# Kernel tuning notes

Measured on AMD Instinct MI355X. Metric: run time of the kernel, lower is better.

Reference implementation:

```python
import jax, jax.numpy as jnp
from jax import lax
import numpy as np

B, C, H, W, O, K = 2, 64, 256, 256, 64, 3
STRIDE, DIL = 1, 1


def setup_inputs() -> dict:
    key = jax.random.key(0)
    ks = jax.random.split(key, 6)
    x = jax.random.normal(ks[0], (B, C, H, W), jnp.float32)
    # offset-predicting conv: 2*k^2 output channels (y,x per kernel tap)
    offset_w = jax.random.normal(ks[1], (2 * K * K, C, K, K), jnp.float32) * 0.01
    offset_b = jax.random.normal(ks[2], (2 * K * K,), jnp.float32) * 0.01
    # modulation conv: k^2 output channels
    amp_w = jax.random.normal(ks[3], (K * K, C, K, K), jnp.float32) * 0.01
    amp_b = jax.random.normal(ks[4], (K * K,), jnp.float32) * 0.01
    # conv3d weight [O, C, 1, 1, k^2] flattened to [O, C, k^2]
    w3d = jax.random.normal(ks[5], (O, C, K * K), jnp.float32) * (1.0 / np.sqrt(C * K * K))
    return {"x": x, "offset_w": offset_w, "offset_b": offset_b,
            "amp_w": amp_w, "amp_b": amp_b, "w3d": w3d}


def _conv2d(inp, w, b):
    out = lax.conv_general_dilated(inp, w, (STRIDE, STRIDE), 'VALID')
    return out + b[None, :, None, None]


def reference(x, offset_w, offset_b, amp_w, amp_b, w3d):
    k2 = K * K
    # 'same' padding as _pad_intput (k=3, s=1, d=1 -> pad 1 each side)
    pfs = K + (K - 1) * (DIL - 1)
    p = pfs - 1
    p0 = p // 2
    pad = jnp.pad(x, ((0, 0), (0, 0), (p0, p - p0), (p0, p - p0)))
    Bb, Cc, in_h, in_w = pad.shape

    off = _conv2d(pad, offset_w, offset_b)          # [B, 2k2, oh, ow]
    oh, ow = off.shape[2], off.shape[3]
    off = off.reshape(Bb, k2, 2, oh, ow).transpose(0, 3, 4, 1, 2)  # [B,oh,ow,k2,2]
    y_off, x_off = off[..., 0], off[..., 1]

    amp = jax.nn.sigmoid(_conv2d(pad, amp_w, amp_b))  # [B, k2, oh, ow]

    # base sampling grid (row-major over (ky,kx), as in nn.Unfold)
    ky, kx = jnp.meshgrid(jnp.arange(K), jnp.arange(K), indexing='ij')
    yb = (jnp.arange(oh) * STRIDE)[:, None] + (ky.reshape(-1) * DIL)[None, :]  # [oh,k2]
    xb = (jnp.arange(ow) * STRIDE)[:, None] + (kx.reshape(-1) * DIL)[None, :]  # [ow,k2]

    y = jnp.clip(yb[None, :, None, :].astype(jnp.float32) + y_off, 0, in_h - 1)
    xx = jnp.clip(xb[None, None, :, :].astype(jnp.float32) + x_off, 0, in_w - 1)
    y0 = jnp.floor(y)
    x0 = jnp.floor(xx)
    y1 = jnp.clip(y0 + 1, 0, in_h - 1)
    x1 = jnp.clip(x0 + 1, 0, in_w - 1)
    y0 = jnp.clip(y0, 0, in_h - 1)
    x0 = jnp.clip(x0, 0, in_w - 1)

    flat = pad.transpose(0, 2, 3, 1).reshape(Bb, in_h * in_w, Cc)

    def gather(yi, xi):
        idx = (yi.astype(jnp.int32) * in_w + xi.astype(jnp.int32)).reshape(Bb, -1)
        return jnp.take_along_axis(flat, idx[:, :, None], axis=1).reshape(Bb, oh, ow, k2, Cc)

    p0g = gather(y0, x0)
    p1g = gather(y0, x1)
    p2g = gather(y1, x0)
    p3g = gather(y1, x1)

    w0 = (y1 - y) * (x1 - xx)
    w1 = (y1 - y) * (xx - x0)
    w2 = (y - y0) * (x1 - xx)
    w3 = (y - y0) * (xx - x0)
    pixels = (w0[..., None] * p0g + w1[..., None] * p1g +
              w2[..., None] * p2g + w3[..., None] * p3g)   # [B,oh,ow,k2,C]

    # sigmoid modulation
    pixels = pixels * amp.transpose(0, 2, 3, 1)[..., None]

    # conv3d (1,1,k^2), no bias: contract over C and k^2
    out = jnp.einsum('bhwkc,ock->bohw', pixels, w3d)
    return jax.nn.relu(out)
```

## Files before the change

### kernel.cpp

```cpp
#include <hip/hip_runtime.h>
#include <hip/hip_bf16.h>
#include <math.h>

#define BB 2
#define CC 64
#define HH 256
#define WW 256
#define OO 64
#define K2 9
#define HW 65536
#define CHW (CC*HW)

typedef _Float16 h8 __attribute__((ext_vector_type(8)));
typedef __fp16 fp16x2 __attribute__((ext_vector_type(2)));
typedef __attribute__((ext_vector_type(4))) unsigned int ux4;
typedef __attribute__((ext_vector_type(4))) float f32x4;

__device__ __forceinline__ int xcd_swz(int bid, int nwg) {
    const int per = nwg >> 3;
    return (bid & 7) * per + (bid >> 3);
}
__device__ __forceinline__ unsigned short f2h(float f) {
    _Float16 h = (_Float16)f;
    return __builtin_bit_cast(unsigned short, h);
}
__device__ __forceinline__ unsigned int pkrtz(float lo, float hi) {
    fp16x2 p = __builtin_amdgcn_cvt_pkrtz(lo, hi);
    return __builtin_bit_cast(unsigned int, p);
}
__device__ __forceinline__ h8 splat8(float f) {
    _Float16 h = (_Float16)f;
    h8 r = {h, h, h, h, h, h, h, h};
    return r;
}

__global__ __launch_bounds__(256) void k_prep(
    const float* __restrict__ offw, const float* __restrict__ ampw,
    const float* __restrict__ w3d,
    unsigned short* __restrict__ wA, unsigned short* __restrict__ wk)
{
    int i = blockIdx.x * 256 + threadIdx.x;
    if (i < 18432) {
        int ch = i / 576, sp = i % 576;
        int tap = sp >> 6, c = sp & 63;
        float v = 0.f;
        if (ch < 18)      v = offw[ch*576 + c*9 + tap];
        else if (ch < 27) v = ampw[(ch-18)*576 + c*9 + tap];
        wA[i] = f2h(v);
    } else if (i < 55296) {
        int j = i - 18432;
        int k = j >> 12, rem = j & 4095;
        int o = rem >> 6, c = rem & 63;
        wk[j] = f2h(w3d[o*576 + c*9 + k]);
    }
}

__global__ __launch_bounds__(256, 3) void k_fused(
    const float* __restrict__ x, const unsigned short* __restrict__ wA,
    const unsigned short* __restrict__ wk,
    const float* __restrict__ offb, const float* __restrict__ ampb,
    float* __restrict__ out)
{
    __shared__ __attribute__((aligned(16))) unsigned char lds[47200];
    unsigned char* tb = lds;
    _Float16* ot16 = (_Float16*)(lds + 43520);

    const int tid = threadIdx.x;
    const int idx = xcd_swz(blockIdx.x, BB*HH*4);
    const int wq = idx & 3, h = (idx >> 2) & 255, b = idx >> 10;
    const int w0 = wq << 6;
    const int lane = tid & 63, wv = tid >> 6;
    const int lrow = lane & 15, lg = lane >> 4;

    const float* xb = x + (size_t)b * CHW;
    const int r0a = h - 2, c0a = w0 - 2;

    {
        auto stage_plane = [&](int pp) {
            const int rr = pp / 68;
            const int cc = pp - rr*68;
            const int ra = r0a + rr, ca = c0a + cc;
            const bool inb = ((unsigned)ra < 256u) && ((unsigned)ca < 256u);
            const float* ps = xb + ra*256 + ca;
            const int swz = (pp & 7) << 4;
            float v[64];
#pragma unroll
            for (int j = 0; j < 64; ++j)
                v[j] = inb ? ps[(size_t)j * HW] : 0.f;
#pragma unroll
            for (int s = 0; s < 8; ++s) {
                ux4 w;
#pragma unroll
                for (int t = 0; t < 4; ++t)
                    w[t] = pkrtz(v[s*8 + 2*t], v[s*8 + 2*t + 1]);
                *(ux4*)(tb + pp*128 + ((s*16) ^ swz)) = w;
            }
        };
        stage_plane(tid);
        if (tid < 340 - 256) stage_plane(tid + 256);
    }
    __syncthreads();

    {
        f32x4 oacc0 = {0.f,0.f,0.f,0.f}, oacc1 = {0.f,0.f,0.f,0.f};
        const int pxl = wv*16 + lrow;
#pragma unroll
        for (int ks = 0; ks < 18; ++ks) {
            const int sbase = ks*32 + lg*8;
            const int tap = sbase >> 6;
            const int cb  = sbase & 63;
            const int ky = tap / 3, kx = tap - ky*3;
            const int pp = (ky + 1)*68 + pxl + kx + 1;
            const h8 bf = *(const h8*)(tb + pp*128 + ((2*cb) ^ ((pp & 7) << 4)));
            const h8 a0 = *(const h8*)(wA + (      lrow)*576 + sbase);
            const h8 a1 = *(const h8*)(wA + (16 + lrow)*576 + sbase);
            oacc0 = __builtin_amdgcn_mfma_f32_16x16x32_f16(a0, bf, oacc0, 0, 0, 0);
            oacc1 = __builtin_amdgcn_mfma_f32_16x16x32_f16(a1, bf, oacc1, 0, 0, 0);
        }
#pragma unroll
        for (int r = 0; r < 4; ++r) {
            int ch0 = lg*4 + r;
            ot16[ch0*68 + pxl] = (_Float16)(oacc0[r] + offb[ch0]);
            int ch1 = 16 + lg*4 + r;
            if (ch1 < 27) {
                float bias = (ch1 < 18) ? offb[ch1] : ampb[ch1 - 18];
                ot16[ch1*68 + pxl] = (_Float16)(oacc1[r] + bias);
            }
        }
    }
    __syncthreads();

    f32x4 acc[4];
#pragma unroll
    for (int n = 0; n < 4; ++n) acc[n] = (f32x4){0.f, 0.f, 0.f, 0.f};

    const int px = wv*16 + lrow;
    const int cA0 = lg*8;
    const int cA1 = 32 + lg*8;
    const int cb0 = lg*16;
    const int cb1 = 64 + lg*16;

#pragma unroll 3
    for (int k = 0; k < K2; ++k) {
        h8 bf0[4], bf1[4];
        {
            const unsigned short* wb = wk + (size_t)k*4096 + lg*8;
#pragma unroll
            for (int n = 0; n < 4; ++n) {
                bf0[n] = *(const h8*)(wb + (n*16 + lrow)*64);
                bf1[n] = *(const h8*)(wb + (n*16 + lrow)*64 + 32);
            }
        }

        const int ky = k / 3, kx = k - ky*3;
        const float oy = (float)ot16[(2*k  )*68 + px];
        const float ox = (float)ot16[(2*k+1)*68 + px];
        const float az = (float)ot16[(18+k )*68 + px];
        float yy = (float)(h + ky) + oy;
        float xx = (float)(w0 + px + kx) + ox;
        yy = fminf(fmaxf(yy, 0.f), 257.f);
        xx = fminf(fmaxf(xx, 0.f), 257.f);
        const float aa = 1.f / (1.f + __expf(-az));

        const float y0f = floorf(yy), x0f = floorf(xx);
        const float y1f = fminf(y0f + 1.f, 257.f);
        const float x1f = fminf(x0f + 1.f, 257.f);
        const float ay = yy - y0f, by = y1f - yy;
        const float ax = xx - x0f, bx = x1f - xx;
        const int r0 = (int)y0f - 1, r1 = (int)y1f - 1;
        const int c0 = (int)x0f - 1, c1 = (int)x1f - 1;
        const int rr0 = r0 - (h - 2), rr1 = r1 - (h - 2);
        const int cc0 = c0 - (w0 - 2), cc1 = c1 - (w0 - 2);
        const float w00 = by*bx*aa, w01 = by*ax*aa, w10 = ay*bx*aa, w11 = ay*ax*aa;

        h8 A0, A1;
        const bool ok = ((unsigned)rr0 <= 4u) && ((unsigned)rr1 <= 4u) &&
                        ((unsigned)cc0 <= 67u) && ((unsigned)cc1 <= 67u);
        if (ok) {
            const int pp00 = rr0*68 + cc0, pp01 = rr0*68 + cc1;
            const int pp10 = rr1*68 + cc0, pp11 = rr1*68 + cc1;
            const int s00 = (pp00 & 7) << 4, s01 = (pp01 & 7) << 4;
            const int s10 = (pp10 & 7) << 4, s11 = (pp11 & 7) << 4;
            const h8 Wb00 = splat8(w00), Wb01 = splat8(w01);
            const h8 Wb10 = splat8(w10), Wb11 = splat8(w11);

            auto bilerp8 = [&](int off) -> h8 {
                const h8 d00 = *(const h8*)(tb + pp00*128 + (off ^ s00));
                const h8 d01 = *(const h8*)(tb + pp01*128 + (off ^ s01));
                const h8 d10 = *(const h8*)(tb + pp10*128 + (off ^ s10));
                const h8 d11 = *(const h8*)(tb + pp11*128 + (off ^ s11));
                h8 t = d00 * Wb00;
                t = __builtin_elementwise_fma(d01, Wb01, t);
                t = __builtin_elementwise_fma(d10, Wb10, t);
                t = __builtin_elementwise_fma(d11, Wb11, t);
                return t;
            };
            A0 = bilerp8(cb0);
            A1 = bilerp8(cb1);
        } else {
            const bool vy0 = (unsigned)r0 < 256u, vy1 = (unsigned)r1 < 256u;
            const bool vx0 = (unsigned)c0 < 256u, vx1 = (unsigned)c1 < 256u;
            float W00 = w00, W01 = w01, W10 = w10, W11 = w11;
            int o00, o01, o10, o11;
            if (vy0 && vx0) o00 = r0*WW + c0; else { o00 = 0; W00 = 0.f; }
            if (vy0 && vx1) o01 = r0*WW + c1; else { o01 = 0; W01 = 0.f; }
            if (vy1 && vx0) o10 = r1*WW + c0; else { o10 = 0; W10 = 0.f; }
            if (vy1 && vx1) o11 = r1*WW + c1; else { o11 = 0; W11 = 0.f; }
            const float* pc0 = xb + (size_t)cA0 * HW;
            const float* pc1 = xb + (size_t)cA1 * HW;
#pragma unroll
            for (int jj = 0; jj < 8; ++jj) {
                float va = W00*pc0[o00] + W01*pc0[o01] + W10*pc0[o10] + W11*pc0[o11];
                pc0 += HW;
                A0[jj] = (_Float16)va;
                float vb = W00*pc1[o00] + W01*pc1[o01] + W10*pc1[o10] + W11*pc1[o11];
                pc1 += HW;
                A1[jj] = (_Float16)vb;
            }
        }

#pragma unroll
        for (int n = 0; n < 4; ++n)
            acc[n] = __builtin_amdgcn_mfma_f32_16x16x32_f16(A0, bf0[n], acc[n], 0, 0, 0);
#pragma unroll
        for (int n = 0; n < 4; ++n)
            acc[n] = __builtin_amdgcn_mfma_f32_16x16x32_f16(A1, bf1[n], acc[n], 0, 0, 0);
    }

    __syncthreads();
    float* ct = (float*)lds;
#pragma unroll
    for (int n = 0; n < 4; ++n)
#pragma unroll
        for (int r = 0; r < 4; ++r)
            ct[(n*16 + lrow)*66 + wv*16 + lg*4 + r] = acc[n][r];
    __syncthreads();

    const size_t ob = (size_t)b*OO*HW + (size_t)h*WW + w0;
#pragma unroll
    for (int it = 0; it < 16; ++it) {
        int o = it*4 + wv;
        out[ob + (size_t)o*HW + lane] = fmaxf(ct[o*66 + lane], 0.f);
    }
}

extern "C" void kernel_launch(void* const* d_in, const int* in_sizes, int n_in,
                              void* d_out, int out_size, void* d_ws, size_t ws_size,
                              hipStream_t stream) {
    const float* x    = (const float*)d_in[0];
    const float* offw = (const float*)d_in[1];
    const float* offb = (const float*)d_in[2];
    const float* ampw = (const float*)d_in[3];
    const float* ampb = (const float*)d_in[4];
    const float* w3d  = (const float*)d_in[5];
    float* out = (float*)d_out;

    unsigned short* wA = (unsigned short*)d_ws;
    unsigned short* wk = wA + 18432;

    k_prep<<<216, 256, 0, stream>>>(offw, ampw, w3d, wA, wk);
    k_fused<<<BB*HH*4, 256, 0, stream>>>(x, wA, wk, offb, ampb, out);
}
```

Baseline: 132.0 us.

## Process two output rows per block and software-pipeline weight fragment loads

Each block now covers a 2x64 output tile with 512 threads instead of 1x64 with 256. The staged halo grows from 5 to 6 rows, so the per-pixel halo traffic from global memory drops, and the bilinear in-tile check is widened to match. The tap loop is restructured to double-buffer the global weight fragments, issuing the next tap's loads before the current tap's compute to hide latency. LDS use and block size both grow, and the launch bound of 512 threads with 4 waves per EU may cap registers and limit occupancy.

```diff
diff --git a/kernel.cpp b/kernel.cpp
--- a/kernel.cpp
+++ b/kernel.cpp
@@ -55,62 +55,59 @@
     }
 }
 
-__global__ __launch_bounds__(256, 3) void k_fused(
+__global__ __launch_bounds__(512, 4) void k_fused(
     const float* __restrict__ x, const unsigned short* __restrict__ wA,
     const unsigned short* __restrict__ wk,
     const float* __restrict__ offb, const float* __restrict__ ampb,
     float* __restrict__ out)
 {
-    __shared__ __attribute__((aligned(16))) unsigned char lds[47200];
+    __shared__ __attribute__((aligned(16))) unsigned char lds[59360];
     unsigned char* tb = lds;
-    _Float16* ot16 = (_Float16*)(lds + 43520);
+    _Float16* ot16 = (_Float16*)(lds + 52224);
 
     const int tid = threadIdx.x;
-    const int idx = xcd_swz(blockIdx.x, BB*HH*4);
-    const int wq = idx & 3, h = (idx >> 2) & 255, b = idx >> 10;
-    const int w0 = wq << 6;
+    const int idx = xcd_swz(blockIdx.x, BB*(HH/2)*4);
+    const int wq = idx & 3, hp = (idx >> 2) & 127, b = idx >> 9;
+    const int h0 = hp << 1, w0 = wq << 6;
     const int lane = tid & 63, wv = tid >> 6;
     const int lrow = lane & 15, lg = lane >> 4;
 
     const float* xb = x + (size_t)b * CHW;
-    const int r0a = h - 2, c0a = w0 - 2;
-
-    {
-        auto stage_plane = [&](int pp) {
-            const int rr = pp / 68;
-            const int cc = pp - rr*68;
-            const int ra = r0a + rr, ca = c0a + cc;
-            const bool inb = ((unsigned)ra < 256u) && ((unsigned)ca < 256u);
-            const float* ps = xb + ra*256 + ca;
-            const int swz = (pp & 7) << 4;
-            float v[64];
-#pragma unroll
-            for (int j = 0; j < 64; ++j)
-                v[j] = inb ? ps[(size_t)j * HW] : 0.f;
-#pragma unroll
-            for (int s = 0; s < 8; ++s) {
-                ux4 w;
-#pragma unroll
-                for (int t = 0; t < 4; ++t)
-                    w[t] = pkrtz(v[s*8 + 2*t], v[s*8 + 2*t + 1]);
-                *(ux4*)(tb + pp*128 + ((s*16) ^ swz)) = w;
-            }
-        };
-        stage_plane(tid);
-        if (tid < 340 - 256) stage_plane(tid + 256);
+    const int r0a = h0 - 2, c0a = w0 - 2;
+
+    if (tid < 408) {
+        const int rr = tid / 68;
+        const int cc = tid - rr*68;
+        const int ra = r0a + rr, ca = c0a + cc;
+        const bool inb = ((unsigned)ra < 256u) && ((unsigned)ca < 256u);
+        const float* ps = xb + ra*256 + ca;
+        const int swz = (tid & 7) << 4;
+        float v[64];
+#pragma unroll
+        for (int j = 0; j < 64; ++j)
+            v[j] = inb ? ps[(size_t)j * HW] : 0.f;
+#pragma unroll
+        for (int s = 0; s < 8; ++s) {
+            ux4 w;
+#pragma unroll
+            for (int t = 0; t < 4; ++t)
+                w[t] = pkrtz(v[s*8 + 2*t], v[s*8 + 2*t + 1]);
+            *(ux4*)(tb + tid*128 + ((s*16) ^ swz)) = w;
+        }
     }
     __syncthreads();
 
     {
         f32x4 oacc0 = {0.f,0.f,0.f,0.f}, oacc1 = {0.f,0.f,0.f,0.f};
         const int pxl = wv*16 + lrow;
+        const int prow = pxl >> 6, pcol = pxl & 63;
 #pragma unroll
         for (int ks = 0; ks < 18; ++ks) {
             const int sbase = ks*32 + lg*8;
             const int tap = sbase >> 6;
             const int cb  = sbase & 63;
             const int ky = tap / 3, kx = tap - ky*3;
-            const int pp = (ky + 1)*68 + pxl + kx + 1;
+            const int pp = (prow + ky + 1)*68 + pcol + kx + 1;
             const h8 bf = *(const h8*)(tb + pp*128 + ((2*cb) ^ ((pp & 7) << 4)));
             const h8 a0 = *(const h8*)(wA + (      lrow)*576 + sbase);
             const h8 a1 = *(const h8*)(wA + (16 + lrow)*576 + sbase);
@@ -120,11 +117,11 @@
 #pragma unroll
         for (int r = 0; r < 4; ++r) {
             int ch0 = lg*4 + r;
-            ot16[ch0*68 + pxl] = (_Float16)(oacc0[r] + offb[ch0]);
+            ot16[ch0*132 + pxl] = (_Float16)(oacc0[r] + offb[ch0]);
             int ch1 = 16 + lg*4 + r;
             if (ch1 < 27) {
                 float bias = (ch1 < 18) ? offb[ch1] : ampb[ch1 - 18];
-                ot16[ch1*68 + pxl] = (_Float16)(oacc1[r] + bias);
+                ot16[ch1*132 + pxl] = (_Float16)(oacc1[r] + bias);
             }
         }
     }
@@ -135,29 +132,28 @@
     for (int n = 0; n < 4; ++n) acc[n] = (f32x4){0.f, 0.f, 0.f, 0.f};
 
     const int px = wv*16 + lrow;
+    const int prow = px >> 6, pcol = px & 63;
     const int cA0 = lg*8;
     const int cA1 = 32 + lg*8;
     const int cb0 = lg*16;
     const int cb1 = 64 + lg*16;
 
-#pragma unroll 3
-    for (int k = 0; k < K2; ++k) {
-        h8 bf0[4], bf1[4];
-        {
-            const unsigned short* wb = wk + (size_t)k*4096 + lg*8;
-#pragma unroll
-            for (int n = 0; n < 4; ++n) {
-                bf0[n] = *(const h8*)(wb + (n*16 + lrow)*64);
-                bf1[n] = *(const h8*)(wb + (n*16 + lrow)*64 + 32);
-            }
-        }
-
+    auto loadB = [&](int k, h8 f0[4], h8 f1[4]) {
+        const unsigned short* wb = wk + (size_t)k*4096 + lg*8;
+#pragma unroll
+        for (int n = 0; n < 4; ++n) {
+            f0[n] = *(const h8*)(wb + (n*16 + lrow)*64);
+            f1[n] = *(const h8*)(wb + (n*16 + lrow)*64 + 32);
+        }
+    };
+
+    auto tap_body = [&](int k, const h8 bf0[4], const h8 bf1[4]) {
         const int ky = k / 3, kx = k - ky*3;
-        const float oy = (float)ot16[(2*k  )*68 + px];
-        const float ox = (float)ot16[(2*k+1)*68 + px];
-        const float az = (float)ot16[(18+k )*68 + px];
-        float yy = (float)(h + ky) + oy;
-        float xx = (float)(w0 + px + kx) + ox;
+        const float oy = (float)ot16[(2*k  )*132 + px];
+        const float ox = (float)ot16[(2*k+1)*132 + px];
+        const float az = (float)ot16[(18+k )*132 + px];
+        float yy = (float)(h0 + prow + ky) + oy;
+        float xx = (float)(w0 + pcol + kx) + ox;
         yy = fminf(fmaxf(yy, 0.f), 257.f);
         xx = fminf(fmaxf(xx, 0.f), 257.f);
         const float aa = 1.f / (1.f + __expf(-az));
@@ -169,12 +165,12 @@
         const float ax = xx - x0f, bx = x1f - xx;
         const int r0 = (int)y0f - 1, r1 = (int)y1f - 1;
         const int c0 = (int)x0f - 1, c1 = (int)x1f - 1;
-        const int rr0 = r0 - (h - 2), rr1 = r1 - (h - 2);
-        const int cc0 = c0 - (w0 - 2), cc1 = c1 - (w0 - 2);
+        const int rr0 = r0 - r0a, rr1 = r1 - r0a;
+        const int cc0 = c0 - c0a, cc1 = c1 - c0a;
         const float w00 = by*bx*aa, w01 = by*ax*aa, w10 = ay*bx*aa, w11 = ay*ax*aa;
 
         h8 A0, A1;
-        const bool ok = ((unsigned)rr0 <= 4u) && ((unsigned)rr1 <= 4u) &&
+        const bool ok = ((unsigned)rr0 <= 5u) && ((unsigned)rr1 <= 5u) &&
                         ((unsigned)cc0 <= 67u) && ((unsigned)cc1 <= 67u);
         if (ok) {
             const int pp00 = rr0*68 + cc0, pp01 = rr0*68 + cc1;
@@ -225,7 +221,18 @@
 #pragma unroll
         for (int n = 0; n < 4; ++n)
             acc[n] = __builtin_amdgcn_mfma_f32_16x16x32_f16(A1, bf1[n], acc[n], 0, 0, 0);
-    }
+    };
+
+    h8 e0[4], e1[4], o0[4], o1[4];
+    loadB(0, e0, e1);
+#pragma unroll 1
+    for (int k = 0; k < 8; k += 2) {
+        loadB(k + 1, o0, o1);
+        tap_body(k, e0, e1);
+        loadB(k + 2, e0, e1);
+        tap_body(k + 1, o0, o1);
+    }
+    tap_body(8, e0, e1);
 
     __syncthreads();
     float* ct = (float*)lds;
@@ -233,14 +240,16 @@
     for (int n = 0; n < 4; ++n)
 #pragma unroll
         for (int r = 0; r < 4; ++r)
-            ct[(n*16 + lrow)*66 + wv*16 + lg*4 + r] = acc[n][r];
-    __syncthreads();
-
-    const size_t ob = (size_t)b*OO*HW + (size_t)h*WW + w0;
+            ct[(n*16 + lrow)*130 + wv*16 + lg*4 + r] = acc[n][r];
+    __syncthreads();
+
+    const size_t ob = (size_t)b*OO*HW + (size_t)h0*WW + w0;
 #pragma unroll
     for (int it = 0; it < 16; ++it) {
-        int o = it*4 + wv;
-        out[ob + (size_t)o*HW + lane] = fmaxf(ct[o*66 + lane], 0.f);
+        const int o = it*4 + (wv & 3);
+        const int row = wv >> 2;
+        out[ob + (size_t)o*HW + row*WW + lane] =
+            fmaxf(ct[o*130 + row*64 + lane], 0.f);
     }
 }
 
@@ -259,5 +268,5 @@
     unsigned short* wk = wA + 18432;
 
     k_prep<<<216, 256, 0, stream>>>(offw, ampw, w3d, wA, wk);
-    k_fused<<<BB*HH*4, 256, 0, stream>>>(x, wA, wk, offb, ampb, out);
-}
+    k_fused<<<BB*(HH/2)*4, 512, 0, stream>>>(x, wA, wk, offb, ampb, out);
+}
```

Result: slower. 171.2 us (+29.7%).

## Split fused kernel into transpose, offset-conv, and gather stages using padded NHWC fp16 copy

Applied to the files above, without the earlier changes.

Adds a pre-pass that transposes x into a zero-padded channels-last fp16 buffer in workspace. The offset/modulation conv becomes its own kernel writing fp16 offsets and sigmoid amplitudes to global memory. The main kernel then gathers bilinear samples straight from the global NHWC buffer with no LDS staging and no out-of-tile fallback path. This removes the per-block strided NCHW loads and the slow fallback path, at the cost of a memset, two extra launches and extra global round trips for the offsets.

```diff
diff --git a/kernel.cpp b/kernel.cpp
--- a/kernel.cpp
+++ b/kernel.cpp
@@ -11,6 +11,18 @@
 #define HW 65536
 #define CHW (CC*HW)
 
+#define XTW 258
+#define XT_ROW (XTW*64)
+#define XT_BATCH (XTW*XTW*64)
+
+#define WA_B   0u
+#define WK_B   36864u
+#define XT_B   110592u
+#define OU_B   17151076u
+#undef OU_B
+#define OU_B   17150976u
+#define AMP_B  21869568u
+
 typedef _Float16 h8 __attribute__((ext_vector_type(8)));
 typedef __fp16 fp16x2 __attribute__((ext_vector_type(2)));
 typedef __attribute__((ext_vector_type(4))) unsigned int ux4;
@@ -24,6 +36,9 @@
     _Float16 h = (_Float16)f;
     return __builtin_bit_cast(unsigned short, h);
 }
+__device__ __forceinline__ float h2f(unsigned short u) {
+    return (float)__builtin_bit_cast(_Float16, u);
+}
 __device__ __forceinline__ unsigned int pkrtz(float lo, float hi) {
     fp16x2 p = __builtin_amdgcn_cvt_pkrtz(lo, hi);
     return __builtin_bit_cast(unsigned int, p);
@@ -34,113 +49,146 @@
     return r;
 }
 
-__global__ __launch_bounds__(256) void k_prep(
-    const float* __restrict__ offw, const float* __restrict__ ampw,
-    const float* __restrict__ w3d,
-    unsigned short* __restrict__ wA, unsigned short* __restrict__ wk)
+__global__ __launch_bounds__(256) void k_pre(
+    const float* __restrict__ x, const float* __restrict__ offw,
+    const float* __restrict__ ampw, const float* __restrict__ w3d,
+    unsigned short* __restrict__ wA, unsigned short* __restrict__ wk,
+    unsigned short* __restrict__ xt)
 {
-    int i = blockIdx.x * 256 + threadIdx.x;
-    if (i < 18432) {
-        int ch = i / 576, sp = i % 576;
-        int tap = sp >> 6, c = sp & 63;
-        float v = 0.f;
-        if (ch < 18)      v = offw[ch*576 + c*9 + tap];
-        else if (ch < 27) v = ampw[(ch-18)*576 + c*9 + tap];
-        wA[i] = f2h(v);
-    } else if (i < 55296) {
-        int j = i - 18432;
-        int k = j >> 12, rem = j & 4095;
-        int o = rem >> 6, c = rem & 63;
-        wk[j] = f2h(w3d[o*576 + c*9 + k]);
-    }
-}
-
-__global__ __launch_bounds__(256, 3) void k_fused(
-    const float* __restrict__ x, const unsigned short* __restrict__ wA,
-    const unsigned short* __restrict__ wk,
+    const int tid = threadIdx.x;
+    const int id = blockIdx.x;
+    if (id < 512) {
+        __shared__ __attribute__((aligned(16))) unsigned char tl[32768];
+        const int b = id >> 8, h = id & 255;
+        const float* xb = x + (size_t)b*CHW + h*256;
+        const int wv = tid >> 6, lane = tid & 63;
+        for (int ip = 0; ip < 8; ++ip) {
+            const int c0 = wv*16 + ip*2;
+            const float* p0 = xb + (size_t)c0*HW;
+#pragma unroll
+            for (int j = 0; j < 4; ++j) {
+                const int px = j*64 + lane;
+                const float v0 = p0[px];
+                const float v1 = p0[HW + px];
+                *(unsigned int*)(tl + px*128 + ((2*c0) ^ ((px & 7) << 4))) =
+                    pkrtz(v0, v1);
+            }
+        }
+        __syncthreads();
+        const int lrow = lane & 15, lg = lane >> 4;
+        unsigned char* rowp = (unsigned char*)(xt + (size_t)b*XT_BATCH +
+                                               (size_t)(h+1)*XT_ROW + 64);
+#pragma unroll
+        for (int g = 0; g < 4; ++g) {
+            const int px = wv*64 + g*16 + lrow;
+            const int swz = (px & 7) << 4;
+            const ux4 a = *(const ux4*)(tl + px*128 + ((lg*16) ^ swz));
+            const ux4 c = *(const ux4*)(tl + px*128 + ((64 + lg*16) ^ swz));
+            *(ux4*)(rowp + (size_t)px*128 + lg*16) = a;
+            *(ux4*)(rowp + (size_t)px*128 + 64 + lg*16) = c;
+        }
+    } else {
+        int i = (id - 512)*256 + tid;
+        if (i < 18432) {
+            int ch = i / 576, sp = i % 576;
+            int tap = sp >> 6, c = sp & 63;
+            float v = 0.f;
+            if (ch < 18)      v = offw[ch*576 + c*9 + tap];
+            else if (ch < 27) v = ampw[(ch-18)*576 + c*9 + tap];
+            wA[i] = f2h(v);
+        } else if (i < 55296) {
+            int j = i - 18432;
+            int k = j >> 12, rem = j & 4095;
+            int o = rem >> 6, c = rem & 63;
+            wk[j] = f2h(w3d[o*576 + c*9 + k]);
+        }
+    }
+}
+
+__global__ __launch_bounds__(256, 4) void k_off(
+    const unsigned short* __restrict__ xt, const unsigned short* __restrict__ wA,
     const float* __restrict__ offb, const float* __restrict__ ampb,
+    unsigned int* __restrict__ ou, unsigned short* __restrict__ amp)
+{
+    const int idx = xcd_swz(blockIdx.x, 2048);
+    const int wq = idx & 3, h = (idx >> 2) & 255, b = idx >> 10;
+    const int w0 = wq << 6;
+    const int lane = threadIdx.x & 63, wv = threadIdx.x >> 6;
+    const int lrow = lane & 15, lg = lane >> 4;
+    const int pxa = w0 + wv*16 + lrow;
+    const unsigned short* xtb = xt + (size_t)b*XT_BATCH;
+
+    f32x4 o0 = {0.f,0.f,0.f,0.f}, o1 = {0.f,0.f,0.f,0.f};
+#pragma unroll
+    for (int ks = 0; ks < 18; ++ks) {
+        const int sbase = ks*32 + lg*8;
+        const int tap = sbase >> 6, cb = sbase & 63;
+        const int ky = tap/3, kx = tap - 3*ky;
+        const h8 bf = *(const h8*)(xtb + (size_t)(h + ky)*XT_ROW +
+                                   (size_t)(pxa + kx)*64 + cb);
+        const h8 a0 = *(const h8*)(wA + lrow*576 + sbase);
+        const h8 a1 = *(const h8*)(wA + (16 + lrow)*576 + sbase);
+        o0 = __builtin_amdgcn_mfma_f32_16x16x32_f16(a0, bf, o0, 0, 0, 0);
+        o1 = __builtin_amdgcn_mfma_f32_16x16x32_f16(a1, bf, o1, 0, 0, 0);
+    }
+    const size_t pix = (size_t)h*256 + pxa;
+    {
+        const int k0 = 2*lg;
+        ou[(size_t)(b*9 + k0    )*HW + pix] =
+            (unsigned int)f2h(o0[0] + offb[4*lg    ]) |
+            ((unsigned int)f2h(o0[1] + offb[4*lg + 1]) << 16);
+        ou[(size_t)(b*9 + k0 + 1)*HW + pix] =
+            (unsigned int)f2h(o0[2] + offb[4*lg + 2]) |
+            ((unsigned int)f2h(o0[3] + offb[4*lg + 3]) << 16);
+        if (lg == 0)
+            ou[(size_t)(b*9 + 8)*HW + pix] =
+                (unsigned int)f2h(o1[0] + offb[16]) |
+                ((unsigned int)f2h(o1[1] + offb[17]) << 16);
+    }
+#pragma unroll
+    for (int r = 0; r < 4; ++r) {
+        const int ch = 16 + lg*4 + r;
+        if (ch >= 18 && ch < 27) {
+            const int k = ch - 18;
+            const float s = 1.f / (1.f + __expf(-(o1[r] + ampb[k])));
+            amp[(size_t)(b*9 + k)*HW + pix] = f2h(s);
+        }
+    }
+}
+
+__global__ __launch_bounds__(256, 4) void k_main(
+    const unsigned short* __restrict__ xt, const unsigned short* __restrict__ wk,
+    const unsigned int* __restrict__ ou, const unsigned short* __restrict__ amp,
     float* __restrict__ out)
 {
-    __shared__ __attribute__((aligned(16))) unsigned char lds[47200];
-    unsigned char* tb = lds;
-    _Float16* ot16 = (_Float16*)(lds + 43520);
-
-    const int tid = threadIdx.x;
-    const int idx = xcd_swz(blockIdx.x, BB*HH*4);
+    __shared__ __attribute__((aligned(16))) float ct[64*66];
+    const int idx = xcd_swz(blockIdx.x, 2048);
     const int wq = idx & 3, h = (idx >> 2) & 255, b = idx >> 10;
     const int w0 = wq << 6;
-    const int lane = tid & 63, wv = tid >> 6;
+    const int lane = threadIdx.x & 63, wv = threadIdx.x >> 6;
     const int lrow = lane & 15, lg = lane >> 4;
-
-    const float* xb = x + (size_t)b * CHW;
-    const int r0a = h - 2, c0a = w0 - 2;
-
-    {
-        auto stage_plane = [&](int pp) {
-            const int rr = pp / 68;
-            const int cc = pp - rr*68;
-            const int ra = r0a + rr, ca = c0a + cc;
-            const bool inb = ((unsigned)ra < 256u) && ((unsigned)ca < 256u);
-            const float* ps = xb + ra*256 + ca;
-            const int swz = (pp & 7) << 4;
-            float v[64];
-#pragma unroll
-            for (int j = 0; j < 64; ++j)
-                v[j] = inb ? ps[(size_t)j * HW] : 0.f;
-#pragma unroll
-            for (int s = 0; s < 8; ++s) {
-                ux4 w;
-#pragma unroll
-                for (int t = 0; t < 4; ++t)
-                    w[t] = pkrtz(v[s*8 + 2*t], v[s*8 + 2*t + 1]);
-                *(ux4*)(tb + pp*128 + ((s*16) ^ swz)) = w;
-            }
-        };
-        stage_plane(tid);
-        if (tid < 340 - 256) stage_plane(tid + 256);
-    }
-    __syncthreads();
-
-    {
-        f32x4 oacc0 = {0.f,0.f,0.f,0.f}, oacc1 = {0.f,0.f,0.f,0.f};
-        const int pxl = wv*16 + lrow;
-#pragma unroll
-        for (int ks = 0; ks < 18; ++ks) {
-            const int sbase = ks*32 + lg*8;
-            const int tap = sbase >> 6;
-            const int cb  = sbase & 63;
-            const int ky = tap / 3, kx = tap - ky*3;
-            const int pp = (ky + 1)*68 + pxl + kx + 1;
-            const h8 bf = *(const h8*)(tb + pp*128 + ((2*cb) ^ ((pp & 7) << 4)));
-            const h8 a0 = *(const h8*)(wA + (      lrow)*576 + sbase);
-            const h8 a1 = *(const h8*)(wA + (16 + lrow)*576 + sbase);
-            oacc0 = __builtin_amdgcn_mfma_f32_16x16x32_f16(a0, bf, oacc0, 0, 0, 0);
-            oacc1 = __builtin_amdgcn_mfma_f32_16x16x32_f16(a1, bf, oacc1, 0, 0, 0);
-        }
-#pragma unroll
-        for (int r = 0; r < 4; ++r) {
-            int ch0 = lg*4 + r;
-            ot16[ch0*68 + pxl] = (_Float16)(oacc0[r] + offb[ch0]);
-            int ch1 = 16 + lg*4 + r;
-            if (ch1 < 27) {
-                float bias = (ch1 < 18) ? offb[ch1] : ampb[ch1 - 18];
-                ot16[ch1*68 + pxl] = (_Float16)(oacc1[r] + bias);
-            }
-        }
-    }
-    __syncthreads();
+    const int pxl = wv*16 + lrow;
+    const int pxa = w0 + pxl;
+    const unsigned char* xtb = (const unsigned char*)(xt + (size_t)b*XT_BATCH);
+    const size_t pix = (size_t)h*256 + pxa;
+
+    float oyv[K2], oxv[K2], aav[K2];
+#pragma unroll
+    for (int k = 0; k < K2; ++k) {
+        const unsigned int u = ou[(size_t)(b*9 + k)*HW + pix];
+        oyv[k] = h2f((unsigned short)(u & 0xffffu));
+        oxv[k] = h2f((unsigned short)(u >> 16));
+        aav[k] = h2f(amp[(size_t)(b*9 + k)*HW + pix]);
+    }
 
     f32x4 acc[4];
 #pragma unroll
     for (int n = 0; n < 4; ++n) acc[n] = (f32x4){0.f, 0.f, 0.f, 0.f};
 
-    const int px = wv*16 + lrow;
-    const int cA0 = lg*8;
-    const int cA1 = 32 + lg*8;
     const int cb0 = lg*16;
     const int cb1 = 64 + lg*16;
 
-#pragma unroll 3
+#pragma unroll
     for (int k = 0; k < K2; ++k) {
         h8 bf0[4], bf1[4];
         {
@@ -152,71 +200,47 @@
             }
         }
 
-        const int ky = k / 3, kx = k - ky*3;
-        const float oy = (float)ot16[(2*k  )*68 + px];
-        const float ox = (float)ot16[(2*k+1)*68 + px];
-        const float az = (float)ot16[(18+k )*68 + px];
-        float yy = (float)(h + ky) + oy;
-        float xx = (float)(w0 + px + kx) + ox;
+        const int ky = k/3, kx = k - 3*ky;
+        float yy = (float)(h + ky) + oyv[k];
+        float xx = (float)(pxa + kx) + oxv[k];
         yy = fminf(fmaxf(yy, 0.f), 257.f);
         xx = fminf(fmaxf(xx, 0.f), 257.f);
-        const float aa = 1.f / (1.f + __expf(-az));
-
         const float y0f = floorf(yy), x0f = floorf(xx);
         const float y1f = fminf(y0f + 1.f, 257.f);
         const float x1f = fminf(x0f + 1.f, 257.f);
         const float ay = yy - y0f, by = y1f - yy;
         const float ax = xx - x0f, bx = x1f - xx;
-        const int r0 = (int)y0f - 1, r1 = (int)y1f - 1;
-        const int c0 = (int)x0f - 1, c1 = (int)x1f - 1;
-        const int rr0 = r0 - (h - 2), rr1 = r1 - (h - 2);
-        const int cc0 = c0 - (w0 - 2), cc1 = c1 - (w0 - 2);
-        const float w00 = by*bx*aa, w01 = by*ax*aa, w10 = ay*bx*aa, w11 = ay*ax*aa;
+        const int y0 = (int)y0f, y1 = (int)y1f;
+        const int x0i = (int)x0f, x1i = (int)x1f;
+        const float aa = aav[k];
+        const h8 W00 = splat8(by*bx*aa), W01 = splat8(by*ax*aa);
+        const h8 W10 = splat8(ay*bx*aa), W11 = splat8(ay*ax*aa);
+
+        const size_t a00 = ((size_t)(y0*XTW + x0i)) * 128;
+        const size_t a01 = ((size_t)(y0*XTW + x1i)) * 128;
+        const size_t a10 = ((size_t)(y1*XTW + x0i)) * 128;
+        const size_t a11 = ((size_t)(y1*XTW + x1i)) * 128;
 
         h8 A0, A1;
-        const bool ok = ((unsigned)rr0 <= 4u) && ((unsigned)rr1 <= 4u) &&
-                        ((unsigned)cc0 <= 67u) && ((unsigned)cc1 <= 67u);
-        if (ok) {
-            const int pp00 = rr0*68 + cc0, pp01 = rr0*68 + cc1;
-            const int pp10 = rr1*68 + cc0, pp11 = rr1*68 + cc1;
-            const int s00 = (pp00 & 7) << 4, s01 = (pp01 & 7) << 4;
-            const int s10 = (pp10 & 7) << 4, s11 = (pp11 & 7) << 4;
-            const h8 Wb00 = splat8(w00), Wb01 = splat8(w01);
-            const h8 Wb10 = splat8(w10), Wb11 = splat8(w11);
-
-            auto bilerp8 = [&](int off) -> h8 {
-                const h8 d00 = *(const h8*)(tb + pp00*128 + (off ^ s00));
-                const h8 d01 = *(const h8*)(tb + pp01*128 + (off ^ s01));
-                const h8 d10 = *(const h8*)(tb + pp10*128 + (off ^ s10));
-                const h8 d11 = *(const h8*)(tb + pp11*128 + (off ^ s11));
-                h8 t = d00 * Wb00;
-                t = __builtin_elementwise_fma(d01, Wb01, t);
-                t = __builtin_elementwise_fma(d10, Wb10, t);
-                t = __builtin_elementwise_fma(d11, Wb11, t);
-                return t;
-            };
-            A0 = bilerp8(cb0);
-            A1 = bilerp8(cb1);
-        } else {
-            const bool vy0 = (unsigned)r0 < 256u, vy1 = (unsigned)r1 < 256u;
-            const bool vx0 = (unsigned)c0 < 256u, vx1 = (unsigned)c1 < 256u;
-            float W00 = w00, W01 = w01, W10 = w10, W11 = w11;
-            int o00, o01, o10, o11;
-            if (vy0 && vx0) o00 = r0*WW + c0; else { o00 = 0; W00 = 0.f; }
-            if (vy0 && vx1) o01 = r0*WW + c1; else { o01 = 0; W01 = 0.f; }
-            if (vy1 && vx0) o10 = r1*WW + c0; else { o10 = 0; W10 = 0.f; }
-            if (vy1 && vx1) o11 = r1*WW + c1; else { o11 = 0; W11 = 0.f; }
-            const float* pc0 = xb + (size_t)cA0 * HW;
-            const float* pc1 = xb + (size_t)cA1 * HW;
-#pragma unroll
-            for (int jj = 0; jj < 8; ++jj) {
-                float va = W00*pc0[o00] + W01*pc0[o01] + W10*pc0[o10] + W11*pc0[o11];
-                pc0 += HW;
-                A0[jj] = (_Float16)va;
-                float vb = W00*pc1[o00] + W01*pc1[o01] + W10*pc1[o10] + W11*pc1[o11];
-                pc1 += HW;
-                A1[jj] = (_Float16)vb;
-            }
+        {
+            const h8 d00 = *(const h8*)(xtb + a00 + cb0);
+            const h8 d01 = *(const h8*)(xtb + a01 + cb0);
+            const h8 d10 = *(const h8*)(xtb + a10 + cb0);
+            const h8 d11 = *(const h8*)(xtb + a11 + cb0);
+            h8 t = d00 * W00;
+            t = __builtin_elementwise_fma(d01, W01, t);
+            t = __builtin_elementwise_fma(d10, W10, t);
+            t = __builtin_elementwise_fma(d11, W11, t);
+            A0 = t;
+            const h8 e00 = *(const h8*)(xtb + a00 + cb1);
+            const h8 e01 = *(const h8*)(xtb + a01 + cb1);
+            const h8 e10 = *(const h8*)(xtb + a10 + cb1);
+            const h8 e11 = *(const h8*)(xtb + a11 + cb1);
+            h8 u = e00 * W00;
+            u = __builtin_elementwise_fma(e01, W01, u);
+            u = __builtin_elementwise_fma(e10, W10, u);
+            u = __builtin_elementwise_fma(e11, W11, u);
+            A1 = u;
         }
 
 #pragma unroll
@@ -227,8 +251,6 @@
             acc[n] = __builtin_amdgcn_mfma_f32_16x16x32_f16(A1, bf1[n], acc[n], 0, 0, 0);
     }
 
-    __syncthreads();
-    float* ct = (float*)lds;
 #pragma unroll
     for (int n = 0; n < 4; ++n)
 #pragma unroll
@@ -239,7 +261,7 @@
     const size_t ob = (size_t)b*OO*HW + (size_t)h*WW + w0;
 #pragma unroll
     for (int it = 0; it < 16; ++it) {
-        int o = it*4 + wv;
+        const int o = it*4 + wv;
         out[ob + (size_t)o*HW + lane] = fmaxf(ct[o*66 + lane], 0.f);
     }
 }
@@ -255,9 +277,15 @@
     const float* w3d  = (const float*)d_in[5];
     float* out = (float*)d_out;
 
-    unsigned short* wA = (unsigned short*)d_ws;
-    unsigned short* wk = wA + 18432;
-
-    k_prep<<<216, 256, 0, stream>>>(offw, ampw, w3d, wA, wk);
-    k_fused<<<BB*HH*4, 256, 0, stream>>>(x, wA, wk, offb, ampb, out);
-}
+    unsigned char* ws = (unsigned char*)d_ws;
+    unsigned short* wA  = (unsigned short*)(ws + WA_B);
+    unsigned short* wk  = (unsigned short*)(ws + WK_B);
+    unsigned short* xt  = (unsigned short*)(ws + XT_B);
+    unsigned int*   ouP = (unsigned int*)(ws + OU_B);
+    unsigned short* amP = (unsigned short*)(ws + AMP_B);
+
+    hipMemsetAsync(xt, 0, (size_t)BB*XT_BATCH*2, stream);
+    k_pre<<<728, 256, 0, stream>>>(x, offw, ampw, w3d, wA, wk, xt);
+    k_off<<<2048, 256, 0, stream>>>(xt, wA, offb, ampb, ouP, amP);
+    k_main<<<2048, 256, 0, stream>>>(xt, wk, ouP, amP, out);
+}
```

Result: slower. 205.0 us (+55.2%).
